# Optimization experiments

Hardware: AMD Instinct MI355X
Metric: run time of the kernel (lower is better)

The kernel has to match this reference:

```python
import jax, jax.numpy as jnp
import numpy as np

B, T, C = 64, 256, 384
H, D = 6, 64  # num_heads, head_size

def setup_inputs() -> dict:
    key = jax.random.key(0)
    ks = jax.random.split(key, 6)
    s = 0.02
    return {
        "x": jax.random.normal(ks[0], (B, T, C), dtype=jnp.float32),
        "Wq": jax.random.normal(ks[1], (H, C, D), dtype=jnp.float32) * s,
        "Wk": jax.random.normal(ks[2], (H, C, D), dtype=jnp.float32) * s,
        "Wv": jax.random.normal(ks[3], (H, C, D), dtype=jnp.float32) * s,
        "Wp": jax.random.normal(ks[4], (C, C), dtype=jnp.float32) * s,
        "bp": jnp.zeros((C,), dtype=jnp.float32),
    }

def reference(x, Wq, Wk, Wv, Wp, bp):
    # per-head projections: [B,T,C] x [H,C,D] -> [B,H,T,D]
    q = jnp.einsum('btc,hcd->bhtd', x, Wq)
    k = jnp.einsum('btc,hcd->bhtd', x, Wk)
    v = jnp.einsum('btc,hcd->bhtd', x, Wv)
    scale = 1.0 / jnp.sqrt(jnp.float32(D))
    scores = jnp.einsum('bhtd,bhsd->bhts', q, k) * scale  # [B,H,T,T]
    Tlen = x.shape[1]
    causal = jnp.tril(jnp.ones((Tlen, Tlen), dtype=bool))
    scores = jnp.where(causal, scores, -jnp.inf)
    wei = jax.nn.softmax(scores, axis=-1)
    # dropout is identity in eval mode
    out = jnp.einsum('bhts,bhsd->bhtd', wei, v)  # [B,H,T,D]
    # concat heads in order (matches torch.cat over head list)
    out = jnp.transpose(out, (0, 2, 1, 3)).reshape(x.shape[0], Tlen, H * D)
    return out @ Wp.T + bp  # nn.Linear: y = x W^T + b
```

## Files before the change

kernel.cpp:

```cpp
#include <hip/hip_runtime.h>

constexpr int Bn = 64, T = 256, C = 384, H = 6, D = 64;
constexpr int BT = Bn * T;
constexpr int NQKV = 3 * C;
constexpr int WALL_ELEMS = NQKV * C;
constexpr int WP_ELEMS = C * C;

using f32x4 = __attribute__((ext_vector_type(4))) float;
using fvec4 = __attribute__((ext_vector_type(4))) float;
using us8   = __attribute__((ext_vector_type(8))) unsigned short;
using bf8   = __attribute__((ext_vector_type(8))) __bf16;

__device__ __forceinline__ unsigned short f2bf(float f) {
  unsigned u = __builtin_bit_cast(unsigned, f);
  u += 0x7FFFu + ((u >> 16) & 1u);
  return (unsigned short)(u >> 16);
}

__device__ __forceinline__ f32x4 mfma16(us8 a, us8 b, f32x4 c) {
  return __builtin_amdgcn_mfma_f32_16x16x32_bf16(
      __builtin_bit_cast(bf8, a), __builtin_bit_cast(bf8, b), c, 0, 0, 0);
}

__global__ __launch_bounds__(256) void k_prep(
    const float* __restrict__ Wq, const float* __restrict__ Wk,
    const float* __restrict__ Wv, unsigned short* __restrict__ Wall) {
  __shared__ unsigned short t[64][71];
  const int bid = blockIdx.x;
  const int ct = bid % 6, ph = bid / 6;
  const int h = ph % 6, p = ph / 6;
  const float* W = (p == 0) ? Wq : (p == 1) ? Wk : Wv;
  const int c0 = ct * 64;
  const int tid = threadIdx.x;
  const int d = tid & 63, cq = tid >> 6;
#pragma unroll
  for (int s = 0; s < 16; ++s) {
    const int c_loc = cq * 16 + s;
    t[c_loc][d] = f2bf(W[(size_t)(h * C + c0 + c_loc) * D + d]);
  }
  __syncthreads();
  const int d_loc = tid >> 2, ch = tid & 3;
#pragma unroll
  for (int it = 0; it < 2; ++it) {
    const int cc = (ch + it * 4) * 8;
    us8 o;
#pragma unroll
    for (int j = 0; j < 8; ++j) o[j] = t[cc + j][d_loc];
    *(us8*)&Wall[(size_t)(p * C + h * D + d_loc) * C + c0 + cc] = o;
  }
}

__global__ __launch_bounds__(256) void k_xcast(
    const float* __restrict__ x, unsigned short* __restrict__ Xb,
    const float* __restrict__ Wp, unsigned short* __restrict__ Wpb) {
  const int i = (blockIdx.x * 256 + threadIdx.x) * 8;
  const float* src;
  unsigned short* dst;
  int off;
  if (i < BT * C) { src = x; dst = Xb; off = i; }
  else { src = Wp; dst = Wpb; off = i - BT * C; }
  fvec4 a = *(const fvec4*)(src + off);
  fvec4 b = *(const fvec4*)(src + off + 4);
  us8 o;
#pragma unroll
  for (int j = 0; j < 4; ++j) { o[j] = f2bf(a[j]); o[4 + j] = f2bf(b[j]); }
  *(us8*)(dst + off) = o;
}

__device__ __forceinline__ void stage_tile(
    const unsigned short* __restrict__ g, unsigned short* l,
    int row0g, int k0, int tr, int tc, int w) {
#pragma unroll
  for (int s = 0; s < 4; ++s) {
    const int row = s * 32 + tr;
    const int sc = (tc ^ (row & 7)) * 8;
    const unsigned short* ga = g + (size_t)(row0g + row) * C + k0 + sc;
    unsigned short* la = l + (s * 32 + w * 8) * 64;
    __builtin_amdgcn_global_load_lds(
        (const __attribute__((address_space(1))) unsigned int*)ga,
        (__attribute__((address_space(3))) unsigned int*)la, 16, 0, 0);
  }
}

template <bool BF16_OUT>
__global__ __launch_bounds__(256) void k_gemm(
    const unsigned short* __restrict__ A,
    const unsigned short* __restrict__ Bm,
    const float* __restrict__ bias,
    unsigned short* __restrict__ Obf, float* __restrict__ Of,
    int Nld, int nwgn) {
  constexpr int BK = 64, NT = C / BK;
  __shared__ unsigned short Al[2][128 * BK];
  __shared__ unsigned short Bl[2][128 * BK];
  const int nwg = gridDim.x;
  const int bid = blockIdx.x;
  const int lin = (bid & 7) * (nwg >> 3) + (bid >> 3);
  const int m0 = (lin / nwgn) * 128, n0 = (lin % nwgn) * 128;
  const int tid = threadIdx.x;
  const int w = tid >> 6, lane = tid & 63;
  const int lr = lane & 15, lg = lane >> 4;
  const int wm = (w >> 1) * 64, wn = (w & 1) * 64;
  const int tr = tid >> 3, tc = tid & 7;

  f32x4 acc[4][4];
#pragma unroll
  for (int i = 0; i < 4; ++i)
#pragma unroll
    for (int j = 0; j < 4; ++j) acc[i][j] = (f32x4){0.f, 0.f, 0.f, 0.f};

  stage_tile(A, &Al[0][0], m0, 0, tr, tc, w);
  stage_tile(Bm, &Bl[0][0], n0, 0, tr, tc, w);
  __syncthreads();

  int cur = 0;
  for (int t = 0; t < NT; ++t) {
    if (t + 1 < NT) {
      stage_tile(A, &Al[cur ^ 1][0], m0, (t + 1) * BK, tr, tc, w);
      stage_tile(Bm, &Bl[cur ^ 1][0], n0, (t + 1) * BK, tr, tc, w);
    }
#pragma unroll
    for (int kc = 0; kc < 2; ++kc) {
      us8 af[4], bfr[4];
#pragma unroll
      for (int i = 0; i < 4; ++i) {
        const int ra = wm + i * 16 + lr;
        af[i] = *(const us8*)&Al[cur][ra * 64 + (((kc * 4 + lg) ^ (ra & 7)) * 8)];
        const int rb = wn + i * 16 + lr;
        bfr[i] = *(const us8*)&Bl[cur][rb * 64 + (((kc * 4 + lg) ^ (rb & 7)) * 8)];
      }
#pragma unroll
      for (int i = 0; i < 4; ++i)
#pragma unroll
        for (int j = 0; j < 4; ++j)
          acc[i][j] = mfma16(af[i], bfr[j], acc[i][j]);
    }
    __syncthreads();
    cur ^= 1;
  }

#pragma unroll
  for (int i = 0; i < 4; ++i)
#pragma unroll
    for (int j = 0; j < 4; ++j) {
      const int col = n0 + wn + j * 16 + lr;
      float bv = BF16_OUT ? 0.f : bias[col];
#pragma unroll
      for (int r = 0; r < 4; ++r) {
        const size_t row = m0 + wm + i * 16 + lg * 4 + r;
        if (BF16_OUT)
          Obf[row * Nld + col] = f2bf(acc[i][j][r]);
        else
          Of[row * Nld + col] = acc[i][j][r] + bv;
      }
    }
}

__global__ __launch_bounds__(512, 4) void k_attn(
    const unsigned short* __restrict__ QKV, unsigned short* __restrict__ Y) {
  __shared__ unsigned short Klds[256][72];
  __shared__ unsigned short Vt[64][264];
  __shared__ unsigned short Pch[8][16][32];
  const int bid = blockIdx.x;
  const int lin = (bid & 7) * 96 + (bid >> 3);
  const int b = lin / 12, rr = lin % 12;
  const int h = rr >> 1, qt = rr & 1;
  const int t0 = qt * 128;
  const int kvlen = t0 + 128;
  const int tid = threadIdx.x;
  const int w = tid >> 6, lane = tid & 63;
  const int lr = lane & 15, lg = lane >> 4;

  {
    const int c8 = (tid & 7) * 8;
    for (int r = tid >> 3; r < kvlen; r += 64) {
      const size_t base = (size_t)(b * T + r) * NQKV + h * D + c8;
      us8 kv = *(const us8*)(QKV + base + C);
      *(us8*)&Klds[r][c8] = kv;
      us8 vv = *(const us8*)(QKV + base + 2 * C);
#pragma unroll
      for (int j = 0; j < 8; ++j) Vt[c8 + j][r] = vv[j];
    }
  }
  __syncthreads();

  const size_t qbase = (size_t)(b * T + t0 + w * 16 + lr) * NQKV + h * D;
  const us8 aq0 = *(const us8*)(QKV + qbase + lg * 8);
  const us8 aq1 = *(const us8*)(QKV + qbase + 32 + lg * 8);

  const int nsf = kvlen / 16;

  f32x4 s[16];
#pragma unroll
  for (int sf = 0; sf < 16; ++sf) s[sf] = (f32x4){0.f, 0.f, 0.f, 0.f};
#pragma unroll
  for (int sf = 0; sf < 16; ++sf) {
    if (sf < nsf) {
      us8 kb0 = *(const us8*)&Klds[sf * 16 + lr][lg * 8];
      s[sf] = mfma16(aq0, kb0, s[sf]);
      us8 kb1 = *(const us8*)&Klds[sf * 16 + lr][32 + lg * 8];
      s[sf] = mfma16(aq1, kb1, s[sf]);
    }
  }

  float mrow[4] = {-1e30f, -1e30f, -1e30f, -1e30f};
#pragma unroll
  for (int sf = 0; sf < 16; ++sf) {
    if (sf < nsf) {
#pragma unroll
      for (int r = 0; r < 4; ++r) {
        const int trow = t0 + w * 16 + lg * 4 + r;
        const int scol = sf * 16 + lr;
        float v = s[sf][r] * 0.125f;
        if (scol > trow) v = -1e30f;
        s[sf][r] = v;
        mrow[r] = fmaxf(mrow[r], v);
      }
    }
  }
#pragma unroll
  for (int dd = 1; dd < 16; dd <<= 1)
#pragma unroll
    for (int r = 0; r < 4; ++r)
      mrow[r] = fmaxf(mrow[r], __shfl_xor(mrow[r], dd, 64));

  float psum[4] = {0.f, 0.f, 0.f, 0.f};
#pragma unroll
  for (int sf = 0; sf < 16; ++sf) {
    if (sf < nsf) {
#pragma unroll
      for (int r = 0; r < 4; ++r) {
        float p = __expf(s[sf][r] - mrow[r]);
        s[sf][r] = p;
        psum[r] += p;
      }
    }
  }
#pragma unroll
  for (int dd = 1; dd < 16; dd <<= 1)
#pragma unroll
    for (int r = 0; r < 4; ++r)
      psum[r] += __shfl_xor(psum[r], dd, 64);

  f32x4 o[4];
#pragma unroll
  for (int nf = 0; nf < 4; ++nf) o[nf] = (f32x4){0.f, 0.f, 0.f, 0.f};
  const int nkk = nsf >> 1;
#pragma unroll
  for (int kk = 0; kk < 8; ++kk) {
    if (kk < nkk) {
#pragma unroll
      for (int half = 0; half < 2; ++half) {
        const int sf = kk * 2 + half;
        const int row = lg * 4;
#pragma unroll
        for (int r = 0; r < 4; ++r) {
          const int cch = (half * 2 + (lr >> 3)) ^ ((row + r) & 3);
          Pch[w][row + r][cch * 8 + (lr & 7)] = f2bf(s[sf][r]);
        }
      }
      __builtin_amdgcn_wave_barrier();
      us8 pa = *(const us8*)&Pch[w][lr][(lg ^ (lr & 3)) * 8];
      __builtin_amdgcn_wave_barrier();
#pragma unroll
      for (int nf = 0; nf < 4; ++nf) {
        us8 bv = *(const us8*)&Vt[nf * 16 + lr][kk * 32 + lg * 8];
        o[nf] = mfma16(pa, bv, o[nf]);
      }
    }
  }

  float rs[4];
#pragma unroll
  for (int r = 0; r < 4; ++r) rs[r] = 1.0f / psum[r];
#pragma unroll
  for (int nf = 0; nf < 4; ++nf)
#pragma unroll
    for (int r = 0; r < 4; ++r) {
      const int trow = t0 + w * 16 + lg * 4 + r;
      Y[(size_t)(b * T + trow) * C + h * D + nf * 16 + lr] =
          f2bf(o[nf][r] * rs[r]);
    }
}

extern "C" void kernel_launch(void* const* d_in, const int* in_sizes, int n_in,
                              void* d_out, int out_size, void* d_ws, size_t ws_size,
                              hipStream_t stream) {
  const float* x  = (const float*)d_in[0];
  const float* Wq = (const float*)d_in[1];
  const float* Wk = (const float*)d_in[2];
  const float* Wv = (const float*)d_in[3];
  const float* Wp = (const float*)d_in[4];
  const float* bp = (const float*)d_in[5];
  float* out = (float*)d_out;

  unsigned short* Wall = (unsigned short*)d_ws;
  unsigned short* Wpb  = Wall + WALL_ELEMS;
  unsigned short* QKV  = Wpb + WP_ELEMS;
  unsigned short* Yb   = QKV + (size_t)BT * NQKV;
  unsigned short* Xb   = Yb;

  k_prep<<<108, 256, 0, stream>>>(Wq, Wk, Wv, Wall);
  k_xcast<<<(BT * C + WP_ELEMS) / (256 * 8), 256, 0, stream>>>(x, Xb, Wp, Wpb);
  k_gemm<true><<<NQKV / 128 * (BT / 128), 256, 0, stream>>>(
      Xb, Wall, nullptr, QKV, nullptr, NQKV, NQKV / 128);
  k_attn<<<T / 128 * H * Bn, 512, 0, stream>>>(QKV, Yb);
  k_gemm<false><<<C / 128 * (BT / 128), 256, 0, stream>>>(
      Yb, Wpb, bp, nullptr, out, C, C / 128);
}
```

Measured before the change: 72.79 us.

## Fuse x cast into QKV GEMM, emit transposed V, async-load K/V in attention

Removes the separate x fp32→bf16 cast kernel: the QKV GEMM now loads x as fp32 from global, converts it in registers and writes swizzled bf16 into LDS, overlapped with the MFMA loop. The V portion of the QKV GEMM output is written directly in a per-head transposed layout, so attention can fill K and V into LDS with global_load_lds using XOR swizzles instead of a scalar transpose. The Wp cast is folded into the weight-prep kernel, and setprio hints are added around the MFMA loops. This saves a launch and an activation round trip, but the A-tile fp32 loads raise register pressure and global traffic in the GEMM.

```diff
diff --git a/kernel.cpp b/kernel.cpp
--- a/kernel.cpp
+++ b/kernel.cpp
@@ -8,6 +8,7 @@
 
 using f32x4 = __attribute__((ext_vector_type(4))) float;
 using fvec4 = __attribute__((ext_vector_type(4))) float;
+using us4   = __attribute__((ext_vector_type(4))) unsigned short;
 using us8   = __attribute__((ext_vector_type(8))) unsigned short;
 using bf8   = __attribute__((ext_vector_type(8))) __bf16;
 
@@ -22,49 +23,50 @@
       __builtin_bit_cast(bf8, a), __builtin_bit_cast(bf8, b), c, 0, 0, 0);
 }
 
+__device__ __forceinline__ void glds16(const unsigned short* g,
+                                       unsigned short* l) {
+  __builtin_amdgcn_global_load_lds(
+      (const __attribute__((address_space(1))) unsigned int*)g,
+      (__attribute__((address_space(3))) unsigned int*)l, 16, 0, 0);
+}
+
 __global__ __launch_bounds__(256) void k_prep(
     const float* __restrict__ Wq, const float* __restrict__ Wk,
-    const float* __restrict__ Wv, unsigned short* __restrict__ Wall) {
+    const float* __restrict__ Wv, const float* __restrict__ Wp,
+    unsigned short* __restrict__ Wall, unsigned short* __restrict__ Wpb) {
   __shared__ unsigned short t[64][71];
   const int bid = blockIdx.x;
-  const int ct = bid % 6, ph = bid / 6;
-  const int h = ph % 6, p = ph / 6;
-  const float* W = (p == 0) ? Wq : (p == 1) ? Wk : Wv;
-  const int c0 = ct * 64;
   const int tid = threadIdx.x;
-  const int d = tid & 63, cq = tid >> 6;
-#pragma unroll
-  for (int s = 0; s < 16; ++s) {
-    const int c_loc = cq * 16 + s;
-    t[c_loc][d] = f2bf(W[(size_t)(h * C + c0 + c_loc) * D + d]);
-  }
-  __syncthreads();
-  const int d_loc = tid >> 2, ch = tid & 3;
-#pragma unroll
-  for (int it = 0; it < 2; ++it) {
-    const int cc = (ch + it * 4) * 8;
+  if (bid < 108) {
+    const int ct = bid % 6, ph = bid / 6;
+    const int h = ph % 6, p = ph / 6;
+    const float* W = (p == 0) ? Wq : (p == 1) ? Wk : Wv;
+    const int c0 = ct * 64;
+    const int d = tid & 63, cq = tid >> 6;
+#pragma unroll
+    for (int s = 0; s < 16; ++s) {
+      const int c_loc = cq * 16 + s;
+      t[c_loc][d] = f2bf(W[(size_t)(h * C + c0 + c_loc) * D + d]);
+    }
+    __syncthreads();
+    const int d_loc = tid >> 2, ch = tid & 3;
+#pragma unroll
+    for (int it = 0; it < 2; ++it) {
+      const int cc = (ch + it * 4) * 8;
+      us8 o;
+#pragma unroll
+      for (int j = 0; j < 8; ++j) o[j] = t[cc + j][d_loc];
+      *(us8*)&Wall[(size_t)(p * C + h * D + d_loc) * C + c0 + cc] = o;
+    }
+  } else {
+    const int off = (bid - 108) * 2048 + tid * 8;
+    fvec4 a = *(const fvec4*)(Wp + off);
+    fvec4 b = *(const fvec4*)(Wp + off + 4);
     us8 o;
 #pragma unroll
-    for (int j = 0; j < 8; ++j) o[j] = t[cc + j][d_loc];
-    *(us8*)&Wall[(size_t)(p * C + h * D + d_loc) * C + c0 + cc] = o;
-  }
-}
-
-__global__ __launch_bounds__(256) void k_xcast(
-    const float* __restrict__ x, unsigned short* __restrict__ Xb,
-    const float* __restrict__ Wp, unsigned short* __restrict__ Wpb) {
-  const int i = (blockIdx.x * 256 + threadIdx.x) * 8;
-  const float* src;
-  unsigned short* dst;
-  int off;
-  if (i < BT * C) { src = x; dst = Xb; off = i; }
-  else { src = Wp; dst = Wpb; off = i - BT * C; }
-  fvec4 a = *(const fvec4*)(src + off);
-  fvec4 b = *(const fvec4*)(src + off + 4);
-  us8 o;
-#pragma unroll
-  for (int j = 0; j < 4; ++j) { o[j] = f2bf(a[j]); o[4 + j] = f2bf(b[j]); }
-  *(us8*)(dst + off) = o;
+    for (int j = 0; j < 4; ++j) { o[j] = f2bf(a[j]); o[4 + j] = f2bf(b[j]); }
+    *(us8*)(Wpb + off) = o;
+  }
 }
 
 __device__ __forceinline__ void stage_tile(
@@ -74,33 +76,139 @@
   for (int s = 0; s < 4; ++s) {
     const int row = s * 32 + tr;
     const int sc = (tc ^ (row & 7)) * 8;
-    const unsigned short* ga = g + (size_t)(row0g + row) * C + k0 + sc;
-    unsigned short* la = l + (s * 32 + w * 8) * 64;
-    __builtin_amdgcn_global_load_lds(
-        (const __attribute__((address_space(1))) unsigned int*)ga,
-        (__attribute__((address_space(3))) unsigned int*)la, 16, 0, 0);
-  }
-}
-
-template <bool BF16_OUT>
-__global__ __launch_bounds__(256) void k_gemm(
-    const unsigned short* __restrict__ A,
-    const unsigned short* __restrict__ Bm,
-    const float* __restrict__ bias,
-    unsigned short* __restrict__ Obf, float* __restrict__ Of,
-    int Nld, int nwgn) {
+    glds16(g + (size_t)(row0g + row) * C + k0 + sc,
+           l + (s * 32 + w * 8) * 64);
+  }
+}
+
+__global__ __launch_bounds__(256) void k_gemm_qkv(
+    const float* __restrict__ X, const unsigned short* __restrict__ Wall,
+    unsigned short* __restrict__ QKV, unsigned short* __restrict__ VT) {
   constexpr int BK = 64, NT = C / BK;
   __shared__ unsigned short Al[2][128 * BK];
   __shared__ unsigned short Bl[2][128 * BK];
   const int nwg = gridDim.x;
   const int bid = blockIdx.x;
   const int lin = (bid & 7) * (nwg >> 3) + (bid >> 3);
-  const int m0 = (lin / nwgn) * 128, n0 = (lin % nwgn) * 128;
+  const int m0 = (lin / 9) * 128, n0 = (lin % 9) * 128;
   const int tid = threadIdx.x;
   const int w = tid >> 6, lane = tid & 63;
   const int lr = lane & 15, lg = lane >> 4;
   const int wm = (w >> 1) * 64, wn = (w & 1) * 64;
   const int tr = tid >> 3, tc = tid & 7;
+  const int ar = tid >> 1, ah = (tid & 1) * 4;
+
+  f32x4 acc[4][4];
+#pragma unroll
+  for (int i = 0; i < 4; ++i)
+#pragma unroll
+    for (int j = 0; j < 4; ++j) acc[i][j] = (f32x4){0.f, 0.f, 0.f, 0.f};
+
+  {
+    const fvec4* gp = (const fvec4*)(X + (size_t)(m0 + ar) * C + (tid & 1) * 32);
+    fvec4 fr[8];
+#pragma unroll
+    for (int j = 0; j < 8; ++j) fr[j] = gp[j];
+    stage_tile(Wall, &Bl[0][0], n0, 0, tr, tc, w);
+#pragma unroll
+    for (int c4 = 0; c4 < 4; ++c4) {
+      us8 o;
+#pragma unroll
+      for (int e = 0; e < 4; ++e) {
+        o[e] = f2bf(fr[2 * c4][e]);
+        o[4 + e] = f2bf(fr[2 * c4 + 1][e]);
+      }
+      *(us8*)&Al[0][ar * 64 + (((ah + c4) ^ (ar & 7)) * 8)] = o;
+    }
+  }
+  __syncthreads();
+
+  int cur = 0;
+  for (int t = 0; t < NT; ++t) {
+    fvec4 fr[8];
+    if (t + 1 < NT) {
+      const fvec4* gp = (const fvec4*)(X + (size_t)(m0 + ar) * C +
+                                       (t + 1) * BK + (tid & 1) * 32);
+#pragma unroll
+      for (int j = 0; j < 8; ++j) fr[j] = gp[j];
+      stage_tile(Wall, &Bl[cur ^ 1][0], n0, (t + 1) * BK, tr, tc, w);
+    }
+#pragma unroll
+    for (int kc = 0; kc < 2; ++kc) {
+      us8 af[4], bfr[4];
+#pragma unroll
+      for (int i = 0; i < 4; ++i) {
+        const int ra = wm + i * 16 + lr;
+        af[i] = *(const us8*)&Al[cur][ra * 64 + (((kc * 4 + lg) ^ (ra & 7)) * 8)];
+        const int rb = wn + i * 16 + lr;
+        bfr[i] = *(const us8*)&Bl[cur][rb * 64 + (((kc * 4 + lg) ^ (rb & 7)) * 8)];
+      }
+#pragma unroll
+      for (int i = 0; i < 4; ++i)
+#pragma unroll
+        for (int j = 0; j < 4; ++j)
+          acc[i][j] = mfma16(af[i], bfr[j], acc[i][j]);
+    }
+    if (t + 1 < NT) {
+#pragma unroll
+      for (int c4 = 0; c4 < 4; ++c4) {
+        us8 o;
+#pragma unroll
+        for (int e = 0; e < 4; ++e) {
+          o[e] = f2bf(fr[2 * c4][e]);
+          o[4 + e] = f2bf(fr[2 * c4 + 1][e]);
+        }
+        *(us8*)&Al[cur ^ 1][ar * 64 + (((ah + c4) ^ (ar & 7)) * 8)] = o;
+      }
+    }
+    __syncthreads();
+    cur ^= 1;
+  }
+
+  if (n0 < 2 * C) {
+#pragma unroll
+    for (int i = 0; i < 4; ++i)
+#pragma unroll
+      for (int j = 0; j < 4; ++j) {
+        const int col = n0 + wn + j * 16 + lr;
+#pragma unroll
+        for (int r = 0; r < 4; ++r) {
+          const size_t row = m0 + wm + i * 16 + lg * 4 + r;
+          QKV[row * NQKV + col] = f2bf(acc[i][j][r]);
+        }
+      }
+  } else {
+#pragma unroll
+    for (int i = 0; i < 4; ++i)
+#pragma unroll
+      for (int j = 0; j < 4; ++j) {
+        const int vcol = n0 + wn + j * 16 + lr - 2 * C;
+        const int h = vcol >> 6, d = vcol & 63;
+        const int row0 = m0 + wm + i * 16 + lg * 4;
+        const int b = row0 >> 8, tq = row0 & 255;
+        us4 o4;
+#pragma unroll
+        for (int r = 0; r < 4; ++r) o4[r] = f2bf(acc[i][j][r]);
+        *(us4*)&VT[(((size_t)b * H + h) * D + d) * T + tq] = o4;
+      }
+  }
+}
+
+__global__ __launch_bounds__(256) void k_gemm_out(
+    const unsigned short* __restrict__ A, const unsigned short* __restrict__ Bm,
+    const float* __restrict__ bias, float* __restrict__ Of) {
+  constexpr int BK = 64, NT = C / BK;
+  __shared__ unsigned short Al[2][128 * BK];
+  __shared__ unsigned short Bl[2][128 * BK];
+  const int nwg = gridDim.x;
+  const int bid = blockIdx.x;
+  const int lin = (bid & 7) * (nwg >> 3) + (bid >> 3);
+  const int m0 = (lin / 3) * 128, n0 = (lin % 3) * 128;
+  const int tid = threadIdx.x;
+  const int w = tid >> 6, lane = tid & 63;
+  const int lr = lane & 15, lg = lane >> 4;
+  const int wm = (w >> 1) * 64, wn = (w & 1) * 64;
+  const int tr = tid >> 3, tc = tid & 7;
 
   f32x4 acc[4][4];
 #pragma unroll
@@ -143,22 +251,20 @@
 #pragma unroll
     for (int j = 0; j < 4; ++j) {
       const int col = n0 + wn + j * 16 + lr;
-      float bv = BF16_OUT ? 0.f : bias[col];
+      const float bv = bias[col];
 #pragma unroll
       for (int r = 0; r < 4; ++r) {
         const size_t row = m0 + wm + i * 16 + lg * 4 + r;
-        if (BF16_OUT)
-          Obf[row * Nld + col] = f2bf(acc[i][j][r]);
-        else
-          Of[row * Nld + col] = acc[i][j][r] + bv;
+        Of[row * C + col] = acc[i][j][r] + bv;
       }
     }
 }
 
 __global__ __launch_bounds__(512, 4) void k_attn(
-    const unsigned short* __restrict__ QKV, unsigned short* __restrict__ Y) {
-  __shared__ unsigned short Klds[256][72];
-  __shared__ unsigned short Vt[64][264];
+    const unsigned short* __restrict__ QKV, const unsigned short* __restrict__ VT,
+    unsigned short* __restrict__ Y) {
+  __shared__ unsigned short Klds[256][64];
+  __shared__ unsigned short Vl[64][256];
   __shared__ unsigned short Pch[8][16][32];
   const int bid = blockIdx.x;
   const int lin = (bid & 7) * 96 + (bid >> 3);
@@ -171,14 +277,20 @@
   const int lr = lane & 15, lg = lane >> 4;
 
   {
-    const int c8 = (tid & 7) * 8;
-    for (int r = tid >> 3; r < kvlen; r += 64) {
-      const size_t base = (size_t)(b * T + r) * NQKV + h * D + c8;
-      us8 kv = *(const us8*)(QKV + base + C);
-      *(us8*)&Klds[r][c8] = kv;
-      us8 vv = *(const us8*)(QKV + base + 2 * C);
-#pragma unroll
-      for (int j = 0; j < 8; ++j) Vt[c8 + j][r] = vv[j];
+    const int rl = lane >> 3, cl = lane & 7;
+    for (int r0 = 0; r0 < kvlen; r0 += 64) {
+      const int row = r0 + w * 8 + rl;
+      glds16(QKV + (size_t)(b * T + row) * NQKV + C + h * D +
+                 ((cl ^ (row & 7)) * 8),
+             &Klds[r0 + w * 8][0]);
+    }
+    const unsigned short* vbase = VT + ((size_t)b * H + h) * D * T;
+    const int dl = lane >> 5, cv = lane & 31;
+#pragma unroll
+    for (int it = 0; it < 4; ++it) {
+      const int d = it * 16 + w * 2 + dl;
+      glds16(vbase + (size_t)d * T + ((cv ^ (d & 7)) * 8),
+             &Vl[it * 16 + w * 2][0]);
     }
   }
   __syncthreads();
@@ -188,19 +300,22 @@
   const us8 aq1 = *(const us8*)(QKV + qbase + 32 + lg * 8);
 
   const int nsf = kvlen / 16;
+  const int xk = lr & 7;
 
   f32x4 s[16];
 #pragma unroll
   for (int sf = 0; sf < 16; ++sf) s[sf] = (f32x4){0.f, 0.f, 0.f, 0.f};
+  __builtin_amdgcn_s_setprio(1);
 #pragma unroll
   for (int sf = 0; sf < 16; ++sf) {
     if (sf < nsf) {
-      us8 kb0 = *(const us8*)&Klds[sf * 16 + lr][lg * 8];
+      us8 kb0 = *(const us8*)&Klds[sf * 16 + lr][(lg ^ xk) * 8];
       s[sf] = mfma16(aq0, kb0, s[sf]);
-      us8 kb1 = *(const us8*)&Klds[sf * 16 + lr][32 + lg * 8];
+      us8 kb1 = *(const us8*)&Klds[sf * 16 + lr][((4 + lg) ^ xk) * 8];
       s[sf] = mfma16(aq1, kb1, s[sf]);
     }
   }
+  __builtin_amdgcn_s_setprio(0);
 
   float mrow[4] = {-1e30f, -1e30f, -1e30f, -1e30f};
 #pragma unroll
@@ -261,11 +376,13 @@
       __builtin_amdgcn_wave_barrier();
       us8 pa = *(const us8*)&Pch[w][lr][(lg ^ (lr & 3)) * 8];
       __builtin_amdgcn_wave_barrier();
+      __builtin_amdgcn_s_setprio(1);
 #pragma unroll
       for (int nf = 0; nf < 4; ++nf) {
-        us8 bv = *(const us8*)&Vt[nf * 16 + lr][kk * 32 + lg * 8];
+        us8 bv = *(const us8*)&Vl[nf * 16 + lr][((kk * 4 + lg) ^ xk) * 8];
         o[nf] = mfma16(pa, bv, o[nf]);
       }
+      __builtin_amdgcn_s_setprio(0);
     }
   }
 
@@ -297,13 +414,10 @@
   unsigned short* Wpb  = Wall + WALL_ELEMS;
   unsigned short* QKV  = Wpb + WP_ELEMS;
   unsigned short* Yb   = QKV + (size_t)BT * NQKV;
-  unsigned short* Xb   = Yb;
-
-  k_prep<<<108, 256, 0, stream>>>(Wq, Wk, Wv, Wall);
-  k_xcast<<<(BT * C + WP_ELEMS) / (256 * 8), 256, 0, stream>>>(x, Xb, Wp, Wpb);
-  k_gemm<true><<<NQKV / 128 * (BT / 128), 256, 0, stream>>>(
-      Xb, Wall, nullptr, QKV, nullptr, NQKV, NQKV / 128);
-  k_attn<<<T / 128 * H * Bn, 512, 0, stream>>>(QKV, Yb);
-  k_gemm<false><<<C / 128 * (BT / 128), 256, 0, stream>>>(
-      Yb, Wpb, bp, nullptr, out, C, C / 128);
-}
+  unsigned short* VT   = Yb + (size_t)BT * C;
+
+  k_prep<<<180, 256, 0, stream>>>(Wq, Wk, Wv, Wp, Wall, Wpb);
+  k_gemm_qkv<<<NQKV / 128 * (BT / 128), 256, 0, stream>>>(x, Wall, QKV, VT);
+  k_attn<<<T / 128 * H * Bn, 512, 0, stream>>>(QKV, VT, Yb);
+  k_gemm_out<<<C / 128 * (BT / 128), 256, 0, stream>>>(Yb, Wpb, bp, out);
+}
```

Result: slower. 92.03 us (+26.4%).
